# Performance work log

Measured on AMD Instinct MI355X. Metric: run time of the kernel, lower is better.

## Reference

```python
import jax, jax.numpy as jnp
import numpy as np

L, B, E = 2048, 4, 1024
H = 8
D1 = 2048          # expand_ratio * E, multiple of H
HD = D1 // H       # head dim 256
MAX_L = 2048
EPS = 1e-8


def setup_inputs() -> dict:
    key = jax.random.key(0)
    ks = jax.random.split(key, 9)
    std = 0.02
    return {
        "x": jax.random.normal(ks[0], (L, B, E), jnp.float32),
        "Wu": jax.random.normal(ks[1], (D1, E), jnp.float32) * std,
        "bu": jax.random.normal(ks[2], (D1,), jnp.float32) * std,
        "Wv": jax.random.normal(ks[3], (D1, E), jnp.float32) * std,
        "bv": jax.random.normal(ks[4], (D1,), jnp.float32) * std,
        "Wo": jax.random.normal(ks[5], (E, D1), jnp.float32) * std,
        "bo": jax.random.normal(ks[6], (E,), jnp.float32) * std,
        "zero": jax.random.normal(ks[7], (H, 1), jnp.float32) * 0.1,   # Toeplitz coef, offset 0
        "pos": jax.random.normal(ks[8], (H, MAX_L - 1), jnp.float32) * 0.1,  # offsets 1..n-1
    }


def _simple_rmsnorm(x):
    d = x.shape[-1]
    rms = jnp.linalg.norm(x, axis=-1, keepdims=True) * (d ** -0.5)
    return x / (rms + EPS)


def _toeplitz_causal_fft(v, zero, pos):
    # v: (b, h, n, hd); causal Toeplitz mixing along n via FFT long conv
    n = v.shape[-2]
    coef = jnp.concatenate([zero, pos[:, : n - 1]], axis=-1)  # (h, n)
    m = 2 * n
    cf = jnp.fft.rfft(coef, m, axis=-1)                  # (h, m//2+1)
    vf = jnp.fft.rfft(v, m, axis=-2)                     # (b, h, m//2+1, hd)
    out = jnp.fft.irfft(cf[None, :, :, None] * vf, m, axis=-2)
    return out[:, :, :n, :]


def reference(x, Wu, bu, Wv, bv, Wo, bo, zero, pos):
    # x: (n, b, e) fairseq layout
    n, b, e = x.shape
    shortcut = x
    xn = _simple_rmsnorm(x)                               # pre_norm (SimpleRMSNorm, no params)
    u = jax.nn.silu(jnp.einsum('nbe,de->nbd', xn, Wu) + bu)   # (n,b,d1)
    v = jax.nn.silu(jnp.einsum('nbe,de->nbd', xn, Wv) + bv)   # (n,b,d1)
    # 'n b (h d) -> b h n d'
    vh = v.transpose(1, 0, 2).reshape(b, n, H, HD).transpose(0, 2, 1, 3)
    oh = _toeplitz_causal_fft(vh, zero, pos)              # (b,h,n,hd)
    o = oh.transpose(0, 2, 1, 3).reshape(b, n, D1).transpose(1, 0, 2)  # (n,b,d1)
    o = u * o                                             # gating
    out = jnp.einsum('nbd,ed->nbe', o, Wo) + bo + shortcut
    return out
```

## Files before the change

kernel.cpp:

```cpp
#include <hip/hip_runtime.h>
#include <cstdint>
#include <cstddef>

#define LQ   2048
#define BQ   4
#define EQ   1024
#define HQ   8
#define D1Q  2048
#define HDQ  256
#define NBQ  (LQ*BQ)

typedef __bf16 bf16_t;
typedef __bf16 bf16x8 __attribute__((ext_vector_type(8)));
typedef __bf16 bf16x4 __attribute__((ext_vector_type(4)));
typedef float  f32x4  __attribute__((ext_vector_type(4)));

#define GAS1(p) ((const __attribute__((address_space(1))) void*)(p))
#define LAS3(p) ((__attribute__((address_space(3))) void*)(p))


__global__ __launch_bounds__(256) void convert_kernel(
    const float* __restrict__ Wu, const float* __restrict__ Wv,
    const float* __restrict__ Wo,
    bf16_t* __restrict__ Wub, bf16_t* __restrict__ Wvb,
    bf16_t* __restrict__ Wob)
{
    const size_t i = (size_t)blockIdx.x * 256 + threadIdx.x;
    if (i < (size_t)D1Q * EQ) {
        Wub[i] = (bf16_t)Wu[i];
        Wvb[i] = (bf16_t)Wv[i];
        Wob[i] = (bf16_t)Wo[i];
    }
}

__global__ __launch_bounds__(256) void build_toep_tiles(
    const float* __restrict__ zero, const float* __restrict__ pos,
    bf16_t* __restrict__ Atiles)
{
    const int q = blockIdx.x;
    const int h = blockIdx.y;
    const int doff = (q - 3) * 32;
    const int tid = threadIdx.x;
    bf16_t* dst = Atiles + ((size_t)h * 64 + q) * (128 * 32);
    const int e0 = tid * 16;
    const int r = e0 >> 5;
    const int cbase = e0 & 31;
    bf16_t vals[16];
    #pragma unroll
    for (int j = 0; j < 16; ++j) {
        const int d = doff + r - (cbase + j);
        float v = 0.f;
        if (d == 0) v = zero[h];
        else if (d > 0) v = pos[(size_t)h * (LQ - 1) + d - 1];
        vals[j] = (bf16_t)v;
    }
    *(bf16x8*)(dst + e0)     = *(bf16x8*)(vals);
    *(bf16x8*)(dst + e0 + 8) = *(bf16x8*)(vals + 8);
}

__global__ __launch_bounds__(256) void rmsnorm_kernel(
    const float* __restrict__ x, bf16_t* __restrict__ xn)
{
    const int row = blockIdx.x;
    const int tid = threadIdx.x;
    const float4 v = ((const float4*)(x + (size_t)row * EQ))[tid];
    float ss = v.x*v.x + v.y*v.y + v.z*v.z + v.w*v.w;
    #pragma unroll
    for (int m = 32; m >= 1; m >>= 1) ss += __shfl_xor(ss, m, 64);
    __shared__ float red[4];
    const int wid = tid >> 6, lane = tid & 63;
    if (lane == 0) red[wid] = ss;
    __syncthreads();
    const float tot = red[0] + red[1] + red[2] + red[3];
    const float inv = 1.f / (sqrtf(tot * (1.f / EQ)) + 1e-8f);
    bf16x4 o;
    o[0] = (bf16_t)(v.x * inv); o[1] = (bf16_t)(v.y * inv);
    o[2] = (bf16_t)(v.z * inv); o[3] = (bf16_t)(v.w * inv);
    *(bf16x4*)(xn + (size_t)row * EQ + tid * 4) = o;
}


template<int MI, int WM, int WN, int MODE, int WPB>
__global__ __launch_bounds__(512, WPB) void gemm_p(
    const bf16_t* __restrict__ A, const bf16_t* __restrict__ Bm,
    int K, int N,
    const float* __restrict__ bias, const float* __restrict__ res,
    bf16_t* __restrict__ Cb, float* __restrict__ Cf)
{
    constexpr int BM = WM * MI * 16;
    constexpr int BN = WN * 64;
    constexpr int ABYTES = BM * 64;
    constexpr int BBYTES = BN * 64;
    constexpr int BSTRIDE = ABYTES + BBYTES;
    constexpr int CB = BN / 128;
    static_assert(BM == 256, "staging assumes BM=256");
    static_assert(MODE != 1 || (MI == 8 && WN == 4), "MODE1 geometry");
    __shared__ alignas(16) char smem[3 * BSTRIDE];

    const int nwg   = gridDim.x * gridDim.y;
    const int bid0  = blockIdx.y * gridDim.x + blockIdx.x;
    const int chunkw = nwg >> 3;
    const int sb    = (bid0 & 7) * chunkw + (bid0 >> 3);
    const int bx    = sb % gridDim.x;
    const int by    = sb / gridDim.x;

    const int tid  = threadIdx.x;
    const int wid  = tid >> 6;
    const int lane = tid & 63;
    const int frow = lane & 15;
    const int c    = lane >> 4;
    const int m0 = by * BM;
    const int n0 = bx * BN;
    const int wm = wid / WN, wn = wid % WN;
    const int wrm = wm * (MI * 16);
    const int wrn = wn * 64;

    const int g = (frow >> 1) & 3;
    const int offA0 = (wrm + frow) * 64 + ((c ^ g) << 4);
    const int offB0 = ABYTES + (wrn + frow) * 64 + ((c ^ g) << 4);

    const int rA   = tid >> 2;
    const int soff = (((tid & 3) ^ ((rA >> 1) & 3)) << 4);
    const size_t lda2 = (size_t)K * 2;
    const char* sA = (const char*)A  + (size_t)(m0 + rA) * lda2 + soff;
    const char* sB = (const char*)Bm + (size_t)(n0 + rA) * lda2 + soff;

    auto STAGE = [&](int bf, int kt) {
        char* dA = smem + bf * BSTRIDE + wid * 1024;
        __builtin_amdgcn_global_load_lds(GAS1(sA + (size_t)kt * 64), LAS3(dA), 16, 0, 0);
        __builtin_amdgcn_global_load_lds(GAS1(sA + 128 * lda2 + (size_t)kt * 64),
                                         LAS3(dA + 8192), 16, 0, 0);
        char* dB = smem + bf * BSTRIDE + ABYTES + wid * 1024;
        __builtin_amdgcn_global_load_lds(GAS1(sB + (size_t)kt * 64), LAS3(dB), 16, 0, 0);
        if constexpr (CB == 2)
            __builtin_amdgcn_global_load_lds(GAS1(sB + 128 * lda2 + (size_t)kt * 64),
                                             LAS3(dB + 8192), 16, 0, 0);
    };

    f32x4 acc[MI][4];
    #pragma unroll
    for (int i = 0; i < MI; ++i)
        #pragma unroll
        for (int j = 0; j < 4; ++j) acc[i][j] = (f32x4){0.f, 0.f, 0.f, 0.f};

    const int NT = K >> 5;

    STAGE(0, 0); STAGE(1, 1);
    if constexpr (CB == 1) asm volatile("s_waitcnt vmcnt(3)" ::: "memory");
    else                   asm volatile("s_waitcnt vmcnt(4)" ::: "memory");
    __builtin_amdgcn_s_barrier();

    int cur = 0, pb = 2;
    for (int t = 0; t < NT; ++t) {
        const char* base = smem + cur * BSTRIDE;
        bf16x8 av[MI], bv[4];
        #pragma unroll
        for (int i = 0; i < MI; ++i)
            av[i] = *(const bf16x8*)(base + offA0 + i * 1024);
        #pragma unroll
        for (int i = 0; i < 4; ++i)
            bv[i] = *(const bf16x8*)(base + offB0 + i * 1024);
        if (t + 2 < NT) STAGE(pb, t + 2);
        __builtin_amdgcn_s_setprio(1);
        #pragma unroll
        for (int mi = 0; mi < MI; ++mi)
            #pragma unroll
            for (int ni = 0; ni < 4; ++ni)
                acc[mi][ni] = __builtin_amdgcn_mfma_f32_16x16x32_bf16(
                    av[mi], bv[ni], acc[mi][ni], 0, 0, 0);
        __builtin_amdgcn_s_setprio(0);
        if (t + 1 < NT) {
            if (t + 2 < NT) {
                if constexpr (CB == 1) asm volatile("s_waitcnt vmcnt(3)" ::: "memory");
                else                   asm volatile("s_waitcnt vmcnt(4)" ::: "memory");
            } else {
                asm volatile("s_waitcnt vmcnt(0)" ::: "memory");
            }
            __builtin_amdgcn_s_barrier();
        }
        cur = (cur == 2) ? 0 : cur + 1;
        pb  = (pb  == 2) ? 0 : pb  + 1;
    }

    if constexpr (MODE == 1) {
        const int hh = n0 >> 8;
        float bb[4];
        #pragma unroll
        for (int ni = 0; ni < 4; ++ni) bb[ni] = bias[n0 + wrn + ni * 16 + frow];

        #pragma unroll
        for (int p = 0; p < 2; ++p) {
            __syncthreads();
            bf16_t* chunk = (bf16_t*)smem + wid * 4224;
            #pragma unroll
            for (int mi = 0; mi < 8; ++mi) {
                #pragma unroll
                for (int nio = 0; nio < 2; ++nio) {
                    const int ni = p * 2 + nio;
                    const int nl = nio * 16 + frow;
                    #pragma unroll
                    for (int j = 0; j < 4; ++j) {
                        float v = acc[mi][ni][j] + bb[ni];
                        v = v / (1.f + __expf(-v));
                        chunk[nl * 132 + j * 32 + mi * 4 + c] = (bf16_t)v;
                    }
                }
            }
            __syncthreads();
            const int nl  = lane & 31;
            const int bh2 = lane >> 5;
            const int hd  = wrn + p * 32 + nl;
            const int t0  = (m0 + wrm) >> 2;
            #pragma unroll
            for (int bi = 0; bi < 2; ++bi) {
                const int b2 = bh2 * 2 + bi;
                const bf16_t* src = chunk + nl * 132 + b2 * 32;
                bf16_t* dst = Cb + (((size_t)hh * 4 + b2) * 256 + hd) * (size_t)LQ + t0;
                #pragma unroll
                for (int q = 0; q < 4; ++q)
                    *(bf16x8*)(dst + q * 8) = *(const bf16x8*)(src + q * 8);
            }
        }
        return;
    }

    const int fq = c * 4;
    #pragma unroll
    for (int mi = 0; mi < MI; ++mi) {
        #pragma unroll
        for (int ni = 0; ni < 4; ++ni) {
            const int gn = n0 + wrn + ni * 16 + frow;
            #pragma unroll
            for (int j = 0; j < 4; ++j) {
                const int gm = m0 + wrm + mi * 16 + fq + j;
                float v = acc[mi][ni][j];
                if constexpr (MODE == 0) {
                    v += bias[gn];
                    v = v / (1.f + __expf(-v));
                    Cb[(size_t)gm * N + gn] = (bf16_t)v;
                } else {
                    v += bias[gn] + res[(size_t)gm * N + gn];
                    Cf[(size_t)gm * N + gn] = v;
                }
            }
        }
    }
}

__global__ __launch_bounds__(512, 2) void gemm_toep_p(
    const bf16_t* __restrict__ VT, const bf16_t* __restrict__ Atiles,
    const bf16_t* __restrict__ U, bf16_t* __restrict__ O)
{
    constexpr int ABYTES = 8192;
    constexpr int BSTRIDE = ABYTES + 16384;
    __shared__ alignas(16) char smem[3 * BSTRIDE];

    const int bid   = blockIdx.x;
    const int m_blk = 15 - (bid >> 5);
    const int sub   = bid & 31;
    const int h     = sub >> 2;
    const int n0    = (sub & 3) * 256;
    const int m0    = m_blk * 128;

    const int tid  = threadIdx.x;
    const int wid  = tid >> 6;
    const int lane = tid & 63;
    const int frow = lane & 15;
    const int c    = lane >> 4;
    const int wrm  = (wid >> 2) * 64;
    const int wrn  = (wid & 3) * 64;

    const int g = (frow >> 1) & 3;
    const int offA0 = (wrm + frow) * 64 + ((c ^ g) << 4);
    const int offB0 = ABYTES + (wrn + frow) * 64 + ((c ^ g) << 4);

    const int rA   = tid >> 2;
    const int soff = (((tid & 3) ^ ((rA >> 1) & 3)) << 4);
    const char* Ah = (const char*)Atiles + (size_t)h * 64 * 8192;
    const size_t ldb = (size_t)LQ * 2;
    const char* sB = (const char*)VT + ((size_t)h * 1024 + n0 + rA) * ldb + soff;

    auto STAGE = [&](int bf, int kt) {
        const int q = 4 * m_blk + 3 - kt;
        __builtin_amdgcn_global_load_lds(
            GAS1(Ah + (size_t)q * 8192 + (size_t)rA * 64 + soff),
            LAS3(smem + bf * BSTRIDE + wid * 1024), 16, 0, 0);
        char* dB = smem + bf * BSTRIDE + ABYTES + wid * 1024;
        __builtin_amdgcn_global_load_lds(GAS1(sB + (size_t)kt * 64), LAS3(dB), 16, 0, 0);
        __builtin_amdgcn_global_load_lds(GAS1(sB + 128 * ldb + (size_t)kt * 64),
                                         LAS3(dB + 8192), 16, 0, 0);
    };

    f32x4 acc[4][4];
    #pragma unroll
    for (int i = 0; i < 4; ++i)
        #pragma unroll
        for (int j = 0; j < 4; ++j) acc[i][j] = (f32x4){0.f, 0.f, 0.f, 0.f};

    const int NT = 4 * m_blk + 4;

    STAGE(0, 0); STAGE(1, 1);
    asm volatile("s_waitcnt vmcnt(3)" ::: "memory");
    __builtin_amdgcn_s_barrier();

    int cur = 0, pb = 2;
    for (int t = 0; t < NT; ++t) {
        const char* base = smem + cur * BSTRIDE;
        bf16x8 av[4], bv[4];
        #pragma unroll
        for (int i = 0; i < 4; ++i)
            av[i] = *(const bf16x8*)(base + offA0 + i * 1024);
        #pragma unroll
        for (int i = 0; i < 4; ++i)
            bv[i] = *(const bf16x8*)(base + offB0 + i * 1024);
        if (t + 2 < NT) STAGE(pb, t + 2);
        __builtin_amdgcn_s_setprio(1);
        #pragma unroll
        for (int mi = 0; mi < 4; ++mi)
            #pragma unroll
            for (int ni = 0; ni < 4; ++ni)
                acc[mi][ni] = __builtin_amdgcn_mfma_f32_16x16x32_bf16(
                    av[mi], bv[ni], acc[mi][ni], 0, 0, 0);
        __builtin_amdgcn_s_setprio(0);
        if (t + 1 < NT) {
            if (t + 2 < NT) asm volatile("s_waitcnt vmcnt(3)" ::: "memory");
            else            asm volatile("s_waitcnt vmcnt(0)" ::: "memory");
            __builtin_amdgcn_s_barrier();
        }
        cur = (cur == 2) ? 0 : cur + 1;
        pb  = (pb  == 2) ? 0 : pb  + 1;
    }

    const int fq = c * 4;
    #pragma unroll
    for (int mi = 0; mi < 4; ++mi) {
        #pragma unroll
        for (int ni = 0; ni < 4; ++ni) {
            const int nn = n0 + wrn + ni * 16 + frow;
            const int b  = nn >> 8, hd = nn & 255;
            #pragma unroll
            for (int j = 0; j < 4; ++j) {
                const int t = m0 + wrm + mi * 16 + fq + j;
                const size_t idx = ((size_t)t * BQ + b) * D1Q + h * HDQ + hd;
                const float uval = (float)U[idx];
                O[idx] = (bf16_t)(uval * acc[mi][ni][j]);
            }
        }
    }
}


extern "C" void kernel_launch(void* const* d_in, const int* in_sizes, int n_in,
                              void* d_out, int out_size, void* d_ws, size_t ws_size,
                              hipStream_t stream)
{
    const float* x    = (const float*)d_in[0];
    const float* Wu   = (const float*)d_in[1];
    const float* bu   = (const float*)d_in[2];
    const float* Wv   = (const float*)d_in[3];
    const float* bv   = (const float*)d_in[4];
    const float* Wo   = (const float*)d_in[5];
    const float* bo   = (const float*)d_in[6];
    const float* zero = (const float*)d_in[7];
    const float* pos  = (const float*)d_in[8];
    float* out = (float*)d_out;

    char* ws = (char*)d_ws;
    size_t off = 0;
    auto alloc = [&](size_t bytes) {
        char* p = ws + off;
        off += (bytes + 255) & ~(size_t)255;
        return p;
    };
    bf16_t* xn     = (bf16_t*)alloc((size_t)NBQ * EQ * 2);
    bf16_t* Wub    = (bf16_t*)alloc((size_t)D1Q * EQ * 2);
    bf16_t* Wvb    = (bf16_t*)alloc((size_t)D1Q * EQ * 2);
    bf16_t* Wob    = (bf16_t*)alloc((size_t)EQ * D1Q * 2);
    bf16_t* Atiles = (bf16_t*)alloc((size_t)HQ * 64 * 4096 * 2);
    bf16_t* Ub     = (bf16_t*)alloc((size_t)NBQ * D1Q * 2);
    bf16_t* VTb    = (bf16_t*)alloc((size_t)NBQ * D1Q * 2);
    bf16_t* Ob     = (bf16_t*)alloc((size_t)NBQ * D1Q * 2);

    convert_kernel<<<8192, 256, 0, stream>>>(Wu, Wv, Wo, Wub, Wvb, Wob);
    build_toep_tiles<<<dim3(64, 8), 256, 0, stream>>>(zero, pos, Atiles);
    rmsnorm_kernel<<<NBQ, 256, 0, stream>>>(x, xn);

    dim3 gU(D1Q / 128, NBQ / 256);
    gemm_p<4, 4, 2, 0, 2><<<gU, 512, 0, stream>>>(xn, Wub, EQ, D1Q, bu, nullptr, Ub, nullptr);
    dim3 gV(D1Q / 256, NBQ / 256);
    gemm_p<8, 2, 4, 1, 1><<<gV, 512, 0, stream>>>(xn, Wvb, EQ, D1Q, bv, nullptr, VTb, nullptr);

    gemm_toep_p<<<512, 512, 0, stream>>>(VTb, Atiles, Ub, Ob);

    dim3 g2(EQ / 128, NBQ / 256);
    gemm_p<4, 4, 2, 2, 2><<<g2, 512, 0, stream>>>(Ob, Wob, D1Q, EQ, bo, x, nullptr, out);
}
```

Before: 206.8 us.

## Restructure GEMM pipelines with 64-wide K tiles and phased prefetch

All four GEMMs now use 64-wide K tiles with an XOR swizzle over 8 chunks. A shared phase_op helper interleaves half-tile LDS loads, asynchronous global-to-LDS staging and MFMA batches with a barrier in each phase. The U and V projections both use a new 256x256 tile kernel with two 64KB buffers. The output projection uses 128x256 tiles, and the Toeplitz tiles are rebuilt as 128x64 blocks so the causal GEMM runs half as many K-steps. The aim is to cut the barrier and waitcnt overhead per unit of MFMA work and to raise reuse per tile, at the cost of much more LDS and one block per CU.

```diff
diff --git a/kernel.cpp b/kernel.cpp
--- a/kernel.cpp
+++ b/kernel.cpp
@@ -33,29 +33,29 @@
     }
 }
 
-__global__ __launch_bounds__(256) void build_toep_tiles(
+__global__ __launch_bounds__(256) void build_toep_tiles2(
     const float* __restrict__ zero, const float* __restrict__ pos,
-    bf16_t* __restrict__ Atiles)
+    bf16_t* __restrict__ At)
 {
     const int q = blockIdx.x;
     const int h = blockIdx.y;
-    const int doff = (q - 3) * 32;
+    const int doff = (q - 1) * 64;
     const int tid = threadIdx.x;
-    bf16_t* dst = Atiles + ((size_t)h * 64 + q) * (128 * 32);
-    const int e0 = tid * 16;
-    const int r = e0 >> 5;
-    const int cbase = e0 & 31;
-    bf16_t vals[16];
-    #pragma unroll
-    for (int j = 0; j < 16; ++j) {
-        const int d = doff + r - (cbase + j);
+    bf16_t* dst = At + ((size_t)h * 32 + q) * 8192;
+    const int r  = tid >> 1;
+    const int c0 = (tid & 1) * 32;
+    bf16_t vals[32];
+    #pragma unroll
+    for (int j = 0; j < 32; ++j) {
+        const int d = doff + r - (c0 + j);
         float v = 0.f;
         if (d == 0) v = zero[h];
-        else if (d > 0) v = pos[(size_t)h * (LQ - 1) + d - 1];
+        else if (d > 0 && d < LQ) v = pos[(size_t)h * (LQ - 1) + d - 1];
         vals[j] = (bf16_t)v;
     }
-    *(bf16x8*)(dst + e0)     = *(bf16x8*)(vals);
-    *(bf16x8*)(dst + e0 + 8) = *(bf16x8*)(vals + 8);
+    #pragma unroll
+    for (int qq = 0; qq < 4; ++qq)
+        *(bf16x8*)(dst + r * 64 + c0 + qq * 8) = *(bf16x8*)(vals + qq * 8);
 }
 
 __global__ __launch_bounds__(256) void rmsnorm_kernel(
@@ -80,22 +80,42 @@
 }
 
 
-template<int MI, int WM, int WN, int MODE, int WPB>
-__global__ __launch_bounds__(512, WPB) void gemm_p(
+template<int KK, int MH, int WAITN, bool LDB, int MI_, typename F>
+__device__ __forceinline__ void phase_op(const char* base, int offA0, int offB0,
+    bf16x8 (&bv)[4], f32x4 (&acc)[MI_][4], F&& stage)
+{
+    bf16x8 av[4];
+    #pragma unroll
+    for (int i = 0; i < 4; ++i)
+        av[i] = *(const bf16x8*)(base + (offA0 ^ (KK << 6)) + (MH * 4 + i) * 2048);
+    if constexpr (LDB) {
+        #pragma unroll
+        for (int i = 0; i < 4; ++i)
+            bv[i] = *(const bf16x8*)(base + (offB0 ^ (KK << 6)) + i * 2048);
+    }
+    stage();
+    __builtin_amdgcn_s_barrier();
+    __builtin_amdgcn_s_setprio(1);
+    #pragma unroll
+    for (int i = 0; i < 4; ++i)
+        #pragma unroll
+        for (int ni = 0; ni < 4; ++ni)
+            acc[MH * 4 + i][ni] = __builtin_amdgcn_mfma_f32_16x16x32_bf16(
+                av[i], bv[ni], acc[MH * 4 + i][ni], 0, 0, 0);
+    __builtin_amdgcn_s_setprio(0);
+    if constexpr (WAITN >= 0)
+        asm volatile("s_waitcnt vmcnt(%0)" :: "i"(WAITN) : "memory");
+    __builtin_amdgcn_s_barrier();
+}
+
+
+template<int MODE>
+__global__ __launch_bounds__(512, 1) void gemm_big(
     const bf16_t* __restrict__ A, const bf16_t* __restrict__ Bm,
-    int K, int N,
-    const float* __restrict__ bias, const float* __restrict__ res,
-    bf16_t* __restrict__ Cb, float* __restrict__ Cf)
-{
-    constexpr int BM = WM * MI * 16;
-    constexpr int BN = WN * 64;
-    constexpr int ABYTES = BM * 64;
-    constexpr int BBYTES = BN * 64;
-    constexpr int BSTRIDE = ABYTES + BBYTES;
-    constexpr int CB = BN / 128;
-    static_assert(BM == 256, "staging assumes BM=256");
-    static_assert(MODE != 1 || (MI == 8 && WN == 4), "MODE1 geometry");
-    __shared__ alignas(16) char smem[3 * BSTRIDE];
+    int K, int N, const float* __restrict__ bias, bf16_t* __restrict__ Cb)
+{
+    constexpr int BSTRIDE = 65536;
+    __shared__ alignas(16) char smem[2 * BSTRIDE];
 
     const int nwg   = gridDim.x * gridDim.y;
     const int bid0  = blockIdx.y * gridDim.x + blockIdx.x;
@@ -109,77 +129,54 @@
     const int lane = tid & 63;
     const int frow = lane & 15;
     const int c    = lane >> 4;
-    const int m0 = by * BM;
-    const int n0 = bx * BN;
-    const int wm = wid / WN, wn = wid % WN;
-    const int wrm = wm * (MI * 16);
-    const int wrn = wn * 64;
-
-    const int g = (frow >> 1) & 3;
-    const int offA0 = (wrm + frow) * 64 + ((c ^ g) << 4);
-    const int offB0 = ABYTES + (wrn + frow) * 64 + ((c ^ g) << 4);
-
-    const int rA   = tid >> 2;
-    const int soff = (((tid & 3) ^ ((rA >> 1) & 3)) << 4);
+    const int m0 = by * 256;
+    const int n0 = bx * 256;
+    const int wrm = (wid >> 2) * 128;
+    const int wrn = (wid & 3) * 64;
+
+    const int g = frow & 7;
+    const int offA0 = (wrm + frow) * 128 + ((c ^ g) << 4);
+    const int offB0 = 32768 + (wrn + frow) * 128 + ((c ^ g) << 4);
+
+    const int rl = tid >> 3;
+    const int ls = (tid & 7) ^ (rl & 7);
     const size_t lda2 = (size_t)K * 2;
-    const char* sA = (const char*)A  + (size_t)(m0 + rA) * lda2 + soff;
-    const char* sB = (const char*)Bm + (size_t)(n0 + rA) * lda2 + soff;
-
-    auto STAGE = [&](int bf, int kt) {
-        char* dA = smem + bf * BSTRIDE + wid * 1024;
-        __builtin_amdgcn_global_load_lds(GAS1(sA + (size_t)kt * 64), LAS3(dA), 16, 0, 0);
-        __builtin_amdgcn_global_load_lds(GAS1(sA + 128 * lda2 + (size_t)kt * 64),
-                                         LAS3(dA + 8192), 16, 0, 0);
-        char* dB = smem + bf * BSTRIDE + ABYTES + wid * 1024;
-        __builtin_amdgcn_global_load_lds(GAS1(sB + (size_t)kt * 64), LAS3(dB), 16, 0, 0);
-        if constexpr (CB == 2)
-            __builtin_amdgcn_global_load_lds(GAS1(sB + 128 * lda2 + (size_t)kt * 64),
-                                             LAS3(dB + 8192), 16, 0, 0);
-    };
-
-    f32x4 acc[MI][4];
-    #pragma unroll
-    for (int i = 0; i < MI; ++i)
+    const char* sA = (const char*)A  + (size_t)(m0 + rl) * lda2 + ls * 16;
+    const char* sB = (const char*)Bm + (size_t)(n0 + rl) * lda2 + ls * 16;
+
+    auto SH = [&](int bf, int op, int hf, int kt) {
+        const char* s = (op ? sB : sA) + (size_t)(hf * 128) * lda2 + (size_t)kt * 128;
+        char* d = smem + bf * BSTRIDE + op * 32768 + hf * 16384 + wid * 1024;
+        __builtin_amdgcn_global_load_lds(GAS1(s), LAS3(d), 16, 0, 0);
+        __builtin_amdgcn_global_load_lds(GAS1(s + 64 * lda2), LAS3(d + 8192), 16, 0, 0);
+    };
+
+    f32x4 acc[8][4];
+    #pragma unroll
+    for (int i = 0; i < 8; ++i)
         #pragma unroll
         for (int j = 0; j < 4; ++j) acc[i][j] = (f32x4){0.f, 0.f, 0.f, 0.f};
-
-    const int NT = K >> 5;
-
-    STAGE(0, 0); STAGE(1, 1);
-    if constexpr (CB == 1) asm volatile("s_waitcnt vmcnt(3)" ::: "memory");
-    else                   asm volatile("s_waitcnt vmcnt(4)" ::: "memory");
+    bf16x8 bv[4];
+
+    const int NT = K >> 6;
+
+    SH(0,0,0,0); SH(0,0,1,0); SH(0,1,0,0); SH(0,1,1,0); SH(1,1,0,1);
+    asm volatile("s_waitcnt vmcnt(2)" ::: "memory");
     __builtin_amdgcn_s_barrier();
 
-    int cur = 0, pb = 2;
-    for (int t = 0; t < NT; ++t) {
-        const char* base = smem + cur * BSTRIDE;
-        bf16x8 av[MI], bv[4];
-        #pragma unroll
-        for (int i = 0; i < MI; ++i)
-            av[i] = *(const bf16x8*)(base + offA0 + i * 1024);
-        #pragma unroll
-        for (int i = 0; i < 4; ++i)
-            bv[i] = *(const bf16x8*)(base + offB0 + i * 1024);
-        if (t + 2 < NT) STAGE(pb, t + 2);
-        __builtin_amdgcn_s_setprio(1);
-        #pragma unroll
-        for (int mi = 0; mi < MI; ++mi)
-            #pragma unroll
-            for (int ni = 0; ni < 4; ++ni)
-                acc[mi][ni] = __builtin_amdgcn_mfma_f32_16x16x32_bf16(
-                    av[mi], bv[ni], acc[mi][ni], 0, 0, 0);
-        __builtin_amdgcn_s_setprio(0);
-        if (t + 1 < NT) {
-            if (t + 2 < NT) {
-                if constexpr (CB == 1) asm volatile("s_waitcnt vmcnt(3)" ::: "memory");
-                else                   asm volatile("s_waitcnt vmcnt(4)" ::: "memory");
-            } else {
-                asm volatile("s_waitcnt vmcnt(0)" ::: "memory");
-            }
-            __builtin_amdgcn_s_barrier();
-        }
-        cur = (cur == 2) ? 0 : cur + 1;
-        pb  = (pb  == 2) ? 0 : pb  + 1;
+    const char* b0 = smem;
+    const char* b1 = smem + BSTRIDE;
+    for (int i = 0; i < NT / 2; ++i) {
+        const int t1 = 2 * i + 1, t2 = 2 * i + 2;
+        const bool p2 = t2 < NT, p3 = t2 + 1 < NT;
+        phase_op<0,0,-1,true >(b0, offA0, offB0, bv, acc, [&]{ SH(1,1,1,t1); });
+        phase_op<0,1,-1,false>(b0, offA0, offB0, bv, acc, [&]{ SH(1,0,0,t1); });
+        phase_op<1,0,-1,true >(b0, offA0, offB0, bv, acc, [&]{ SH(1,0,1,t1); });
+        phase_op<1,1, 2,false>(b0, offA0, offB0, bv, acc, [&]{ if (p2) SH(0,1,0,t2); });
+        phase_op<0,0,-1,true >(b1, offA0, offB0, bv, acc, [&]{ if (p2) SH(0,1,1,t2); });
+        phase_op<0,1,-1,false>(b1, offA0, offB0, bv, acc, [&]{ if (p2) SH(0,0,0,t2); });
+        phase_op<1,0,-1,true >(b1, offA0, offB0, bv, acc, [&]{ if (p2) SH(0,0,1,t2); });
+        phase_op<1,1, 2,false>(b1, offA0, offB0, bv, acc, [&]{ if (p3) SH(1,1,0,t2+1); });
     }
 
     if constexpr (MODE == 1) {
@@ -226,33 +223,118 @@
 
     const int fq = c * 4;
     #pragma unroll
-    for (int mi = 0; mi < MI; ++mi) {
+    for (int mi = 0; mi < 8; ++mi) {
         #pragma unroll
         for (int ni = 0; ni < 4; ++ni) {
             const int gn = n0 + wrn + ni * 16 + frow;
             #pragma unroll
             for (int j = 0; j < 4; ++j) {
                 const int gm = m0 + wrm + mi * 16 + fq + j;
-                float v = acc[mi][ni][j];
-                if constexpr (MODE == 0) {
-                    v += bias[gn];
-                    v = v / (1.f + __expf(-v));
-                    Cb[(size_t)gm * N + gn] = (bf16_t)v;
-                } else {
-                    v += bias[gn] + res[(size_t)gm * N + gn];
-                    Cf[(size_t)gm * N + gn] = v;
-                }
+                float v = acc[mi][ni][j] + bias[gn];
+                v = v / (1.f + __expf(-v));
+                Cb[(size_t)gm * N + gn] = (bf16_t)v;
             }
         }
     }
 }
 
-__global__ __launch_bounds__(512, 2) void gemm_toep_p(
-    const bf16_t* __restrict__ VT, const bf16_t* __restrict__ Atiles,
+__global__ __launch_bounds__(512, 1) void gemm_fin(
+    const bf16_t* __restrict__ A, const bf16_t* __restrict__ Bm,
+    const float* __restrict__ bias, const float* __restrict__ res,
+    float* __restrict__ Cf)
+{
+    constexpr int K = D1Q, N = EQ;
+    constexpr int BSTRIDE = 49152;
+    __shared__ alignas(16) char smem[3 * BSTRIDE];
+
+    const int nwg   = gridDim.x * gridDim.y;
+    const int bid0  = blockIdx.y * gridDim.x + blockIdx.x;
+    const int chunkw = nwg >> 3;
+    const int sb    = (bid0 & 7) * chunkw + (bid0 >> 3);
+    const int bx    = sb % gridDim.x;
+    const int by    = sb / gridDim.x;
+
+    const int tid  = threadIdx.x;
+    const int wid  = tid >> 6;
+    const int lane = tid & 63;
+    const int frow = lane & 15;
+    const int c    = lane >> 4;
+    const int m0 = by * 128;
+    const int n0 = bx * 256;
+    const int wrm = (wid >> 2) * 64;
+    const int wrn = (wid & 3) * 64;
+
+    const int g = frow & 7;
+    const int offA0 = (wrm + frow) * 128 + ((c ^ g) << 4);
+    const int offB0 = 16384 + (wrn + frow) * 128 + ((c ^ g) << 4);
+
+    const int rl = tid >> 3;
+    const int ls = (tid & 7) ^ (rl & 7);
+    const size_t lda2 = (size_t)K * 2;
+    const char* sA = (const char*)A  + (size_t)(m0 + rl) * lda2 + ls * 16;
+    const char* sB = (const char*)Bm + (size_t)(n0 + rl) * lda2 + ls * 16;
+
+    auto SH_A = [&](int bf, int kt) {
+        const char* s = sA + (size_t)kt * 128;
+        char* d = smem + bf * BSTRIDE + wid * 1024;
+        __builtin_amdgcn_global_load_lds(GAS1(s), LAS3(d), 16, 0, 0);
+        __builtin_amdgcn_global_load_lds(GAS1(s + 64 * lda2), LAS3(d + 8192), 16, 0, 0);
+    };
+    auto SH_B = [&](int bf, int hf, int kt) {
+        const char* s = sB + (size_t)(hf * 128) * lda2 + (size_t)kt * 128;
+        char* d = smem + bf * BSTRIDE + 16384 + hf * 16384 + wid * 1024;
+        __builtin_amdgcn_global_load_lds(GAS1(s), LAS3(d), 16, 0, 0);
+        __builtin_amdgcn_global_load_lds(GAS1(s + 64 * lda2), LAS3(d + 8192), 16, 0, 0);
+    };
+
+    f32x4 acc[4][4];
+    #pragma unroll
+    for (int i = 0; i < 4; ++i)
+        #pragma unroll
+        for (int j = 0; j < 4; ++j) acc[i][j] = (f32x4){0.f, 0.f, 0.f, 0.f};
+    bf16x8 bv[4];
+
+    const int NT = K >> 6;
+
+    SH_A(0, 0); SH_B(0, 0, 0); SH_B(0, 1, 0);
+    SH_A(1, 1); SH_B(1, 0, 1); SH_B(1, 1, 1);
+    asm volatile("s_waitcnt vmcnt(6)" ::: "memory");
+    __builtin_amdgcn_s_barrier();
+
+    int cur = 0, pb = 2;
+    for (int t = 0; t < NT; ++t) {
+        const char* base = smem + cur * BSTRIDE;
+        const int t2 = t + 2;
+        const bool pf = t2 < NT;
+        phase_op<0,0,-1,true>(base, offA0, offB0, bv, acc,
+            [&]{ if (pf) { SH_A(pb, t2); SH_B(pb, 0, t2); } });
+        phase_op<1,0, 6,true>(base, offA0, offB0, bv, acc,
+            [&]{ if (pf) SH_B(pb, 1, t2); });
+        cur = (cur == 2) ? 0 : cur + 1;
+        pb  = (pb  == 2) ? 0 : pb  + 1;
+    }
+
+    const int fq = c * 4;
+    #pragma unroll
+    for (int mi = 0; mi < 4; ++mi) {
+        #pragma unroll
+        for (int ni = 0; ni < 4; ++ni) {
+            const int gn = n0 + wrn + ni * 16 + frow;
+            #pragma unroll
+            for (int j = 0; j < 4; ++j) {
+                const int gm = m0 + wrm + mi * 16 + fq + j;
+                Cf[(size_t)gm * N + gn] =
+                    acc[mi][ni][j] + bias[gn] + res[(size_t)gm * N + gn];
+            }
+        }
+    }
+}
+
+__global__ __launch_bounds__(512, 1) void gemm_toep4p(
+    const bf16_t* __restrict__ VT, const bf16_t* __restrict__ Atl,
     const bf16_t* __restrict__ U, bf16_t* __restrict__ O)
 {
-    constexpr int ABYTES = 8192;
-    constexpr int BSTRIDE = ABYTES + 16384;
+    constexpr int BSTRIDE = 49152;
     __shared__ alignas(16) char smem[3 * BSTRIDE];
 
     const int bid   = blockIdx.x;
@@ -270,25 +352,28 @@
     const int wrm  = (wid >> 2) * 64;
     const int wrn  = (wid & 3) * 64;
 
-    const int g = (frow >> 1) & 3;
-    const int offA0 = (wrm + frow) * 64 + ((c ^ g) << 4);
-    const int offB0 = ABYTES + (wrn + frow) * 64 + ((c ^ g) << 4);
-
-    const int rA   = tid >> 2;
-    const int soff = (((tid & 3) ^ ((rA >> 1) & 3)) << 4);
-    const char* Ah = (const char*)Atiles + (size_t)h * 64 * 8192;
+    const int g = frow & 7;
+    const int offA0 = (wrm + frow) * 128 + ((c ^ g) << 4);
+    const int offB0 = 16384 + (wrn + frow) * 128 + ((c ^ g) << 4);
+
+    const int rl = tid >> 3;
+    const int ls = (tid & 7) ^ (rl & 7);
+    const char* Ah = (const char*)Atl + (size_t)h * 32 * 16384;
     const size_t ldb = (size_t)LQ * 2;
-    const char* sB = (const char*)VT + ((size_t)h * 1024 + n0 + rA) * ldb + soff;
-
-    auto STAGE = [&](int bf, int kt) {
-        const int q = 4 * m_blk + 3 - kt;
-        __builtin_amdgcn_global_load_lds(
-            GAS1(Ah + (size_t)q * 8192 + (size_t)rA * 64 + soff),
-            LAS3(smem + bf * BSTRIDE + wid * 1024), 16, 0, 0);
-        char* dB = smem + bf * BSTRIDE + ABYTES + wid * 1024;
-        __builtin_amdgcn_global_load_lds(GAS1(sB + (size_t)kt * 64), LAS3(dB), 16, 0, 0);
-        __builtin_amdgcn_global_load_lds(GAS1(sB + 128 * ldb + (size_t)kt * 64),
-                                         LAS3(dB + 8192), 16, 0, 0);
+    const char* sB = (const char*)VT + ((size_t)h * 1024 + n0 + rl) * ldb + ls * 16;
+
+    auto SH_A = [&](int bf, int kt) {
+        const int q = 2 * m_blk - kt + 1;
+        const char* s = Ah + (size_t)q * 16384 + (size_t)rl * 128 + ls * 16;
+        char* d = smem + bf * BSTRIDE + wid * 1024;
+        __builtin_amdgcn_global_load_lds(GAS1(s), LAS3(d), 16, 0, 0);
+        __builtin_amdgcn_global_load_lds(GAS1(s + 64 * 128), LAS3(d + 8192), 16, 0, 0);
+    };
+    auto SH_B = [&](int bf, int hf, int kt) {
+        const char* s = sB + (size_t)(hf * 128) * ldb + (size_t)kt * 128;
+        char* d = smem + bf * BSTRIDE + 16384 + hf * 16384 + wid * 1024;
+        __builtin_amdgcn_global_load_lds(GAS1(s), LAS3(d), 16, 0, 0);
+        __builtin_amdgcn_global_load_lds(GAS1(s + 64 * ldb), LAS3(d + 8192), 16, 0, 0);
     };
 
     f32x4 acc[4][4];
@@ -296,37 +381,24 @@
     for (int i = 0; i < 4; ++i)
         #pragma unroll
         for (int j = 0; j < 4; ++j) acc[i][j] = (f32x4){0.f, 0.f, 0.f, 0.f};
-
-    const int NT = 4 * m_blk + 4;
-
-    STAGE(0, 0); STAGE(1, 1);
-    asm volatile("s_waitcnt vmcnt(3)" ::: "memory");
+    bf16x8 bv[4];
+
+    const int NT = 2 * m_blk + 2;
+
+    SH_A(0, 0); SH_B(0, 0, 0); SH_B(0, 1, 0);
+    SH_A(1, 1); SH_B(1, 0, 1); SH_B(1, 1, 1);
+    asm volatile("s_waitcnt vmcnt(6)" ::: "memory");
     __builtin_amdgcn_s_barrier();
 
     int cur = 0, pb = 2;
     for (int t = 0; t < NT; ++t) {
         const char* base = smem + cur * BSTRIDE;
-        bf16x8 av[4], bv[4];
-        #pragma unroll
-        for (int i = 0; i < 4; ++i)
-            av[i] = *(const bf16x8*)(base + offA0 + i * 1024);
-        #pragma unroll
-        for (int i = 0; i < 4; ++i)
-            bv[i] = *(const bf16x8*)(base + offB0 + i * 1024);
-        if (t + 2 < NT) STAGE(pb, t + 2);
-        __builtin_amdgcn_s_setprio(1);
-        #pragma unroll
-        for (int mi = 0; mi < 4; ++mi)
-            #pragma unroll
-            for (int ni = 0; ni < 4; ++ni)
-                acc[mi][ni] = __builtin_amdgcn_mfma_f32_16x16x32_bf16(
-                    av[mi], bv[ni], acc[mi][ni], 0, 0, 0);
-        __builtin_amdgcn_s_setprio(0);
-        if (t + 1 < NT) {
-            if (t + 2 < NT) asm volatile("s_waitcnt vmcnt(3)" ::: "memory");
-            else            asm volatile("s_waitcnt vmcnt(0)" ::: "memory");
-            __builtin_amdgcn_s_barrier();
-        }
+        const int t2 = t + 2;
+        const bool pf = t2 < NT;
+        phase_op<0,0,-1,true>(base, offA0, offB0, bv, acc,
+            [&]{ if (pf) { SH_A(pb, t2); SH_B(pb, 0, t2); } });
+        phase_op<1,0, 6,true>(base, offA0, offB0, bv, acc,
+            [&]{ if (pf) SH_B(pb, 1, t2); });
         cur = (cur == 2) ? 0 : cur + 1;
         pb  = (pb  == 2) ? 0 : pb  + 1;
     }
@@ -376,22 +448,21 @@
     bf16_t* Wub    = (bf16_t*)alloc((size_t)D1Q * EQ * 2);
     bf16_t* Wvb    = (bf16_t*)alloc((size_t)D1Q * EQ * 2);
     bf16_t* Wob    = (bf16_t*)alloc((size_t)EQ * D1Q * 2);
-    bf16_t* Atiles = (bf16_t*)alloc((size_t)HQ * 64 * 4096 * 2);
+    bf16_t* Atiles = (bf16_t*)alloc((size_t)HQ * 32 * 8192 * 2);
     bf16_t* Ub     = (bf16_t*)alloc((size_t)NBQ * D1Q * 2);
     bf16_t* VTb    = (bf16_t*)alloc((size_t)NBQ * D1Q * 2);
     bf16_t* Ob     = (bf16_t*)alloc((size_t)NBQ * D1Q * 2);
 
     convert_kernel<<<8192, 256, 0, stream>>>(Wu, Wv, Wo, Wub, Wvb, Wob);
-    build_toep_tiles<<<dim3(64, 8), 256, 0, stream>>>(zero, pos, Atiles);
+    build_toep_tiles2<<<dim3(32, 8), 256, 0, stream>>>(zero, pos, Atiles);
     rmsnorm_kernel<<<NBQ, 256, 0, stream>>>(x, xn);
 
-    dim3 gU(D1Q / 128, NBQ / 256);
-    gemm_p<4, 4, 2, 0, 2><<<gU, 512, 0, stream>>>(xn, Wub, EQ, D1Q, bu, nullptr, Ub, nullptr);
-    dim3 gV(D1Q / 256, NBQ / 256);
-    gemm_p<8, 2, 4, 1, 1><<<gV, 512, 0, stream>>>(xn, Wvb, EQ, D1Q, bv, nullptr, VTb, nullptr);
-
-    gemm_toep_p<<<512, 512, 0, stream>>>(VTb, Atiles, Ub, Ob);
-
-    dim3 g2(EQ / 128, NBQ / 256);
-    gemm_p<4, 4, 2, 2, 2><<<g2, 512, 0, stream>>>(Ob, Wob, D1Q, EQ, bo, x, nullptr, out);
-}
+    dim3 g1(D1Q / 256, NBQ / 256);
+    gemm_big<0><<<g1, 512, 0, stream>>>(xn, Wub, EQ, D1Q, bu, Ub);
+    gemm_big<1><<<g1, 512, 0, stream>>>(xn, Wvb, EQ, D1Q, bv, VTb);
+
+    gemm_toep4p<<<512, 512, 0, stream>>>(VTb, Atiles, Ub, Ob);
+
+    dim3 g2(EQ / 256, NBQ / 128);
+    gemm_fin<<<g2, 512, 0, stream>>>(Ob, Wob, bo, x, out);
+}
```

Measured after the change: 198.2 us. 4.2% less time.

## Merge U/V projections into one GEMM launch and shrink tiles with double buffering

Applied to the files above, without the earlier changes.

The two input-projection GEMMs become a single launch. Its grid spans both weight matrices, relying on Wvb sitting contiguously after Wub in the workspace, and the epilogue branches per block to write either gated U or transposed V. The Toeplitz and output GEMMs move from 512-thread 256-wide tiles to 256-thread 128x128 tiles, doubling the number of blocks and raising the occupancy hint. All GEMMs switch from a three-stage LDS pipeline to two stages with a full vmcnt(0) wait every iteration. This aims for better load balance and more resident blocks, at the cost of shallower prefetch and more redundant operand loads from the smaller tiles.

```diff
diff --git a/kernel.cpp b/kernel.cpp
--- a/kernel.cpp
+++ b/kernel.cpp
@@ -79,23 +79,14 @@
     *(bf16x4*)(xn + (size_t)row * EQ + tid * 4) = o;
 }
 
-
-template<int MI, int WM, int WN, int MODE, int WPB>
-__global__ __launch_bounds__(512, WPB) void gemm_p(
+__global__ __launch_bounds__(512, 4) void gemm_uv(
     const bf16_t* __restrict__ A, const bf16_t* __restrict__ Bm,
-    int K, int N,
-    const float* __restrict__ bias, const float* __restrict__ res,
-    bf16_t* __restrict__ Cb, float* __restrict__ Cf)
-{
-    constexpr int BM = WM * MI * 16;
-    constexpr int BN = WN * 64;
-    constexpr int ABYTES = BM * 64;
-    constexpr int BBYTES = BN * 64;
-    constexpr int BSTRIDE = ABYTES + BBYTES;
-    constexpr int CB = BN / 128;
-    static_assert(BM == 256, "staging assumes BM=256");
-    static_assert(MODE != 1 || (MI == 8 && WN == 4), "MODE1 geometry");
-    __shared__ alignas(16) char smem[3 * BSTRIDE];
+    const float* __restrict__ bbu, const float* __restrict__ bbv,
+    bf16_t* __restrict__ Ub, bf16_t* __restrict__ Vt)
+{
+    constexpr int K = EQ;
+    constexpr int BUF = 24576;
+    __shared__ alignas(16) char smem[2 * BUF];
 
     const int nwg   = gridDim.x * gridDim.y;
     const int bid0  = blockIdx.y * gridDim.x + blockIdx.x;
@@ -109,15 +100,14 @@
     const int lane = tid & 63;
     const int frow = lane & 15;
     const int c    = lane >> 4;
-    const int m0 = by * BM;
-    const int n0 = bx * BN;
-    const int wm = wid / WN, wn = wid % WN;
-    const int wrm = wm * (MI * 16);
-    const int wrn = wn * 64;
+    const int m0 = by * 256;
+    const int n0 = bx * 128;
+    const int wm = wid >> 1, wn = wid & 1;
+    const int wrm = wm * 64, wrn = wn * 64;
 
     const int g = (frow >> 1) & 3;
     const int offA0 = (wrm + frow) * 64 + ((c ^ g) << 4);
-    const int offB0 = ABYTES + (wrn + frow) * 64 + ((c ^ g) << 4);
+    const int offB0 = 16384 + (wrn + frow) * 64 + ((c ^ g) << 4);
 
     const int rA   = tid >> 2;
     const int soff = (((tid & 3) ^ ((rA >> 1) & 3)) << 4);
@@ -126,140 +116,120 @@
     const char* sB = (const char*)Bm + (size_t)(n0 + rA) * lda2 + soff;
 
     auto STAGE = [&](int bf, int kt) {
-        char* dA = smem + bf * BSTRIDE + wid * 1024;
+        char* dA = smem + bf * BUF + wid * 1024;
         __builtin_amdgcn_global_load_lds(GAS1(sA + (size_t)kt * 64), LAS3(dA), 16, 0, 0);
         __builtin_amdgcn_global_load_lds(GAS1(sA + 128 * lda2 + (size_t)kt * 64),
                                          LAS3(dA + 8192), 16, 0, 0);
-        char* dB = smem + bf * BSTRIDE + ABYTES + wid * 1024;
+        char* dB = smem + bf * BUF + 16384 + wid * 1024;
         __builtin_amdgcn_global_load_lds(GAS1(sB + (size_t)kt * 64), LAS3(dB), 16, 0, 0);
-        if constexpr (CB == 2)
-            __builtin_amdgcn_global_load_lds(GAS1(sB + 128 * lda2 + (size_t)kt * 64),
-                                             LAS3(dB + 8192), 16, 0, 0);
     };
 
-    f32x4 acc[MI][4];
-    #pragma unroll
-    for (int i = 0; i < MI; ++i)
+    f32x4 acc[4][4];
+    #pragma unroll
+    for (int i = 0; i < 4; ++i)
         #pragma unroll
         for (int j = 0; j < 4; ++j) acc[i][j] = (f32x4){0.f, 0.f, 0.f, 0.f};
 
     const int NT = K >> 5;
 
-    STAGE(0, 0); STAGE(1, 1);
-    if constexpr (CB == 1) asm volatile("s_waitcnt vmcnt(3)" ::: "memory");
-    else                   asm volatile("s_waitcnt vmcnt(4)" ::: "memory");
+    STAGE(0, 0);
+    asm volatile("s_waitcnt vmcnt(0)" ::: "memory");
     __builtin_amdgcn_s_barrier();
 
-    int cur = 0, pb = 2;
     for (int t = 0; t < NT; ++t) {
-        const char* base = smem + cur * BSTRIDE;
-        bf16x8 av[MI], bv[4];
-        #pragma unroll
-        for (int i = 0; i < MI; ++i)
+        if (t + 1 < NT) STAGE((t + 1) & 1, t + 1);
+        const char* base = smem + (t & 1) * BUF;
+        bf16x8 av[4], bv[4];
+        #pragma unroll
+        for (int i = 0; i < 4; ++i) {
             av[i] = *(const bf16x8*)(base + offA0 + i * 1024);
-        #pragma unroll
-        for (int i = 0; i < 4; ++i)
             bv[i] = *(const bf16x8*)(base + offB0 + i * 1024);
-        if (t + 2 < NT) STAGE(pb, t + 2);
+        }
         __builtin_amdgcn_s_setprio(1);
         #pragma unroll
-        for (int mi = 0; mi < MI; ++mi)
+        for (int mi = 0; mi < 4; ++mi)
             #pragma unroll
             for (int ni = 0; ni < 4; ++ni)
                 acc[mi][ni] = __builtin_amdgcn_mfma_f32_16x16x32_bf16(
                     av[mi], bv[ni], acc[mi][ni], 0, 0, 0);
         __builtin_amdgcn_s_setprio(0);
-        if (t + 1 < NT) {
-            if (t + 2 < NT) {
-                if constexpr (CB == 1) asm volatile("s_waitcnt vmcnt(3)" ::: "memory");
-                else                   asm volatile("s_waitcnt vmcnt(4)" ::: "memory");
-            } else {
-                asm volatile("s_waitcnt vmcnt(0)" ::: "memory");
+        asm volatile("s_waitcnt vmcnt(0)" ::: "memory");
+        __builtin_amdgcn_s_barrier();
+    }
+
+    if (bx < 16) {
+        const int fq = c * 4;
+        #pragma unroll
+        for (int mi = 0; mi < 4; ++mi) {
+            #pragma unroll
+            for (int ni = 0; ni < 4; ++ni) {
+                const int gn = n0 + wrn + ni * 16 + frow;
+                #pragma unroll
+                for (int j = 0; j < 4; ++j) {
+                    const int gm = m0 + wrm + mi * 16 + fq + j;
+                    float v = acc[mi][ni][j] + bbu[gn];
+                    v = v / (1.f + __expf(-v));
+                    Ub[(size_t)gm * D1Q + gn] = (bf16_t)v;
+                }
             }
-            __builtin_amdgcn_s_barrier();
-        }
-        cur = (cur == 2) ? 0 : cur + 1;
-        pb  = (pb  == 2) ? 0 : pb  + 1;
-    }
-
-    if constexpr (MODE == 1) {
-        const int hh = n0 >> 8;
+        }
+        return;
+    }
+
+    {
+        const int n0v = n0 - 2048;
+        const int hh  = n0v >> 8;
+        const int hdb = (n0v & 255) + wrn;
         float bb[4];
         #pragma unroll
-        for (int ni = 0; ni < 4; ++ni) bb[ni] = bias[n0 + wrn + ni * 16 + frow];
-
+        for (int ni = 0; ni < 4; ++ni) bb[ni] = bbv[n0v + wrn + ni * 16 + frow];
+
+        bf16_t* chunk = (bf16_t*)smem + wn * 8448;
         #pragma unroll
         for (int p = 0; p < 2; ++p) {
             __syncthreads();
-            bf16_t* chunk = (bf16_t*)smem + wid * 4224;
-            #pragma unroll
-            for (int mi = 0; mi < 8; ++mi) {
+            #pragma unroll
+            for (int mi = 0; mi < 4; ++mi) {
                 #pragma unroll
                 for (int nio = 0; nio < 2; ++nio) {
                     const int ni = p * 2 + nio;
                     const int nl = nio * 16 + frow;
+                    const int tl = wm * 16 + mi * 4 + c;
                     #pragma unroll
                     for (int j = 0; j < 4; ++j) {
                         float v = acc[mi][ni][j] + bb[ni];
                         v = v / (1.f + __expf(-v));
-                        chunk[nl * 132 + j * 32 + mi * 4 + c] = (bf16_t)v;
+                        chunk[nl * 264 + j * 64 + tl] = (bf16_t)v;
                     }
                 }
             }
             __syncthreads();
-            const int nl  = lane & 31;
-            const int bh2 = lane >> 5;
-            const int hd  = wrn + p * 32 + nl;
-            const int t0  = (m0 + wrm) >> 2;
-            #pragma unroll
-            for (int bi = 0; bi < 2; ++bi) {
-                const int b2 = bh2 * 2 + bi;
-                const bf16_t* src = chunk + nl * 132 + b2 * 32;
-                bf16_t* dst = Cb + (((size_t)hh * 4 + b2) * 256 + hd) * (size_t)LQ + t0;
-                #pragma unroll
-                for (int q = 0; q < 4; ++q)
-                    *(bf16x8*)(dst + q * 8) = *(const bf16x8*)(src + q * 8);
-            }
-        }
-        return;
-    }
-
-    const int fq = c * 4;
-    #pragma unroll
-    for (int mi = 0; mi < MI; ++mi) {
-        #pragma unroll
-        for (int ni = 0; ni < 4; ++ni) {
-            const int gn = n0 + wrn + ni * 16 + frow;
-            #pragma unroll
-            for (int j = 0; j < 4; ++j) {
-                const int gm = m0 + wrm + mi * 16 + fq + j;
-                float v = acc[mi][ni][j];
-                if constexpr (MODE == 0) {
-                    v += bias[gn];
-                    v = v / (1.f + __expf(-v));
-                    Cb[(size_t)gm * N + gn] = (bf16_t)v;
-                } else {
-                    v += bias[gn] + res[(size_t)gm * N + gn];
-                    Cf[(size_t)gm * N + gn] = v;
-                }
-            }
-        }
-    }
-}
-
-__global__ __launch_bounds__(512, 2) void gemm_toep_p(
+            const int nl    = lane & 31;
+            const int thalf = lane >> 5;
+            const int b2    = wm;
+            const int hd    = hdb + p * 32 + nl;
+            const int t0    = (m0 >> 2) + thalf * 32;
+            const bf16_t* src = chunk + nl * 264 + b2 * 64 + thalf * 32;
+            bf16_t* dst = Vt + (((size_t)hh * 4 + b2) * 256 + hd) * (size_t)LQ + t0;
+            #pragma unroll
+            for (int u = 0; u < 4; ++u)
+                *(bf16x8*)(dst + u * 8) = *(const bf16x8*)(src + u * 8);
+        }
+    }
+}
+
+__global__ __launch_bounds__(256, 4) void gemm_toep(
     const bf16_t* __restrict__ VT, const bf16_t* __restrict__ Atiles,
     const bf16_t* __restrict__ U, bf16_t* __restrict__ O)
 {
-    constexpr int ABYTES = 8192;
-    constexpr int BSTRIDE = ABYTES + 16384;
-    __shared__ alignas(16) char smem[3 * BSTRIDE];
+    constexpr int BUF = 16384;
+    __shared__ alignas(16) char smem[2 * BUF];
 
     const int bid   = blockIdx.x;
-    const int m_blk = 15 - (bid >> 5);
-    const int sub   = bid & 31;
-    const int h     = sub >> 2;
-    const int n0    = (sub & 3) * 256;
+    const int m_blk = 15 - (bid >> 6);
+    const int sub   = bid & 63;
+    const int h     = sub >> 3;
+    const int n0    = (sub & 7) * 128;
     const int m0    = m_blk * 128;
 
     const int tid  = threadIdx.x;
@@ -267,12 +237,12 @@
     const int lane = tid & 63;
     const int frow = lane & 15;
     const int c    = lane >> 4;
-    const int wrm  = (wid >> 2) * 64;
-    const int wrn  = (wid & 3) * 64;
+    const int wm = wid >> 1, wn = wid & 1;
+    const int wrm = wm * 64, wrn = wn * 64;
 
     const int g = (frow >> 1) & 3;
     const int offA0 = (wrm + frow) * 64 + ((c ^ g) << 4);
-    const int offB0 = ABYTES + (wrn + frow) * 64 + ((c ^ g) << 4);
+    const int offB0 = 8192 + (wrn + frow) * 64 + ((c ^ g) << 4);
 
     const int rA   = tid >> 2;
     const int soff = (((tid & 3) ^ ((rA >> 1) & 3)) << 4);
@@ -282,13 +252,14 @@
 
     auto STAGE = [&](int bf, int kt) {
         const int q = 4 * m_blk + 3 - kt;
-        __builtin_amdgcn_global_load_lds(
-            GAS1(Ah + (size_t)q * 8192 + (size_t)rA * 64 + soff),
-            LAS3(smem + bf * BSTRIDE + wid * 1024), 16, 0, 0);
-        char* dB = smem + bf * BSTRIDE + ABYTES + wid * 1024;
+        const char* s = Ah + (size_t)q * 8192 + (size_t)rA * 64 + soff;
+        char* dA = smem + bf * BUF + wid * 1024;
+        __builtin_amdgcn_global_load_lds(GAS1(s), LAS3(dA), 16, 0, 0);
+        __builtin_amdgcn_global_load_lds(GAS1(s + 4096), LAS3(dA + 4096), 16, 0, 0);
+        char* dB = smem + bf * BUF + 8192 + wid * 1024;
         __builtin_amdgcn_global_load_lds(GAS1(sB + (size_t)kt * 64), LAS3(dB), 16, 0, 0);
-        __builtin_amdgcn_global_load_lds(GAS1(sB + 128 * ldb + (size_t)kt * 64),
-                                         LAS3(dB + 8192), 16, 0, 0);
+        __builtin_amdgcn_global_load_lds(GAS1(sB + 64 * ldb + (size_t)kt * 64),
+                                         LAS3(dB + 4096), 16, 0, 0);
     };
 
     f32x4 acc[4][4];
@@ -299,21 +270,19 @@
 
     const int NT = 4 * m_blk + 4;
 
-    STAGE(0, 0); STAGE(1, 1);
-    asm volatile("s_waitcnt vmcnt(3)" ::: "memory");
+    STAGE(0, 0);
+    asm volatile("s_waitcnt vmcnt(0)" ::: "memory");
     __builtin_amdgcn_s_barrier();
 
-    int cur = 0, pb = 2;
     for (int t = 0; t < NT; ++t) {
-        const char* base = smem + cur * BSTRIDE;
+        if (t + 1 < NT) STAGE((t + 1) & 1, t + 1);
+        const char* base = smem + (t & 1) * BUF;
         bf16x8 av[4], bv[4];
         #pragma unroll
-        for (int i = 0; i < 4; ++i)
+        for (int i = 0; i < 4; ++i) {
             av[i] = *(const bf16x8*)(base + offA0 + i * 1024);
-        #pragma unroll
-        for (int i = 0; i < 4; ++i)
             bv[i] = *(const bf16x8*)(base + offB0 + i * 1024);
-        if (t + 2 < NT) STAGE(pb, t + 2);
+        }
         __builtin_amdgcn_s_setprio(1);
         #pragma unroll
         for (int mi = 0; mi < 4; ++mi)
@@ -322,13 +291,8 @@
                 acc[mi][ni] = __builtin_amdgcn_mfma_f32_16x16x32_bf16(
                     av[mi], bv[ni], acc[mi][ni], 0, 0, 0);
         __builtin_amdgcn_s_setprio(0);
-        if (t + 1 < NT) {
-            if (t + 2 < NT) asm volatile("s_waitcnt vmcnt(3)" ::: "memory");
-            else            asm volatile("s_waitcnt vmcnt(0)" ::: "memory");
-            __builtin_amdgcn_s_barrier();
-        }
-        cur = (cur == 2) ? 0 : cur + 1;
-        pb  = (pb  == 2) ? 0 : pb  + 1;
+        asm volatile("s_waitcnt vmcnt(0)" ::: "memory");
+        __builtin_amdgcn_s_barrier();
     }
 
     const int fq = c * 4;
@@ -344,6 +308,102 @@
                 const size_t idx = ((size_t)t * BQ + b) * D1Q + h * HDQ + hd;
                 const float uval = (float)U[idx];
                 O[idx] = (bf16_t)(uval * acc[mi][ni][j]);
+            }
+        }
+    }
+}
+
+__global__ __launch_bounds__(256, 4) void gemm_fin(
+    const bf16_t* __restrict__ A, const bf16_t* __restrict__ Bm,
+    const float* __restrict__ bias, const float* __restrict__ res,
+    float* __restrict__ Cf)
+{
+    constexpr int K = D1Q, N = EQ;
+    constexpr int BUF = 16384;
+    __shared__ alignas(16) char smem[2 * BUF];
+
+    const int nwg   = gridDim.x * gridDim.y;
+    const int bid0  = blockIdx.y * gridDim.x + blockIdx.x;
+    const int chunkw = nwg >> 3;
+    const int sb    = (bid0 & 7) * chunkw + (bid0 >> 3);
+    const int bx    = sb % gridDim.x;
+    const int by    = sb / gridDim.x;
+
+    const int tid  = threadIdx.x;
+    const int wid  = tid >> 6;
+    const int lane = tid & 63;
+    const int frow = lane & 15;
+    const int c    = lane >> 4;
+    const int m0 = by * 128;
+    const int n0 = bx * 128;
+    const int wm = wid >> 1, wn = wid & 1;
+    const int wrm = wm * 64, wrn = wn * 64;
+
+    const int g = (frow >> 1) & 3;
+    const int offA0 = (wrm + frow) * 64 + ((c ^ g) << 4);
+    const int offB0 = 8192 + (wrn + frow) * 64 + ((c ^ g) << 4);
+
+    const int rA   = tid >> 2;
+    const int soff = (((tid & 3) ^ ((rA >> 1) & 3)) << 4);
+    const size_t lda2 = (size_t)K * 2;
+    const char* sA = (const char*)A  + (size_t)(m0 + rA) * lda2 + soff;
+    const char* sB = (const char*)Bm + (size_t)(n0 + rA) * lda2 + soff;
+
+    auto STAGE = [&](int bf, int kt) {
+        char* dA = smem + bf * BUF + wid * 1024;
+        __builtin_amdgcn_global_load_lds(GAS1(sA + (size_t)kt * 64), LAS3(dA), 16, 0, 0);
+        __builtin_amdgcn_global_load_lds(GAS1(sA + 64 * lda2 + (size_t)kt * 64),
+                                         LAS3(dA + 4096), 16, 0, 0);
+        char* dB = smem + bf * BUF + 8192 + wid * 1024;
+        __builtin_amdgcn_global_load_lds(GAS1(sB + (size_t)kt * 64), LAS3(dB), 16, 0, 0);
+        __builtin_amdgcn_global_load_lds(GAS1(sB + 64 * lda2 + (size_t)kt * 64),
+                                         LAS3(dB + 4096), 16, 0, 0);
+    };
+
+    f32x4 acc[4][4];
+    #pragma unroll
+    for (int i = 0; i < 4; ++i)
+        #pragma unroll
+        for (int j = 0; j < 4; ++j) acc[i][j] = (f32x4){0.f, 0.f, 0.f, 0.f};
+
+    const int NT = K >> 5;
+
+    STAGE(0, 0);
+    asm volatile("s_waitcnt vmcnt(0)" ::: "memory");
+    __builtin_amdgcn_s_barrier();
+
+    for (int t = 0; t < NT; ++t) {
+        if (t + 1 < NT) STAGE((t + 1) & 1, t + 1);
+        const char* base = smem + (t & 1) * BUF;
+        bf16x8 av[4], bv[4];
+        #pragma unroll
+        for (int i = 0; i < 4; ++i) {
+            av[i] = *(const bf16x8*)(base + offA0 + i * 1024);
+            bv[i] = *(const bf16x8*)(base + offB0 + i * 1024);
+        }
+        __builtin_amdgcn_s_setprio(1);
+        #pragma unroll
+        for (int mi = 0; mi < 4; ++mi)
+            #pragma unroll
+            for (int ni = 0; ni < 4; ++ni)
+                acc[mi][ni] = __builtin_amdgcn_mfma_f32_16x16x32_bf16(
+                    av[mi], bv[ni], acc[mi][ni], 0, 0, 0);
+        __builtin_amdgcn_s_setprio(0);
+        asm volatile("s_waitcnt vmcnt(0)" ::: "memory");
+        __builtin_amdgcn_s_barrier();
+    }
+
+    const int fq = c * 4;
+    #pragma unroll
+    for (int mi = 0; mi < 4; ++mi) {
+        #pragma unroll
+        for (int ni = 0; ni < 4; ++ni) {
+            const int gn = n0 + wrn + ni * 16 + frow;
+            #pragma unroll
+            for (int j = 0; j < 4; ++j) {
+                const int gm = m0 + wrm + mi * 16 + fq + j;
+                Cf[(size_t)gm * N + gn] =
+                    acc[mi][ni][j] + bias[gn] + res[(size_t)gm * N + gn];
             }
         }
     }
@@ -385,13 +445,11 @@
     build_toep_tiles<<<dim3(64, 8), 256, 0, stream>>>(zero, pos, Atiles);
     rmsnorm_kernel<<<NBQ, 256, 0, stream>>>(x, xn);
 
-    dim3 gU(D1Q / 128, NBQ / 256);
-    gemm_p<4, 4, 2, 0, 2><<<gU, 512, 0, stream>>>(xn, Wub, EQ, D1Q, bu, nullptr, Ub, nullptr);
-    dim3 gV(D1Q / 256, NBQ / 256);
-    gemm_p<8, 2, 4, 1, 1><<<gV, 512, 0, stream>>>(xn, Wvb, EQ, D1Q, bv, nullptr, VTb, nullptr);
-
-    gemm_toep_p<<<512, 512, 0, stream>>>(VTb, Atiles, Ub, Ob);
-
-    dim3 g2(EQ / 128, NBQ / 256);
-    gemm_p<4, 4, 2, 2, 2><<<g2, 512, 0, stream>>>(Ob, Wob, D1Q, EQ, bo, x, nullptr, out);
-}
+    dim3 g1(32, NBQ / 256);
+    gemm_uv<<<g1, 512, 0, stream>>>(xn, Wub, bu, bv, Ub, VTb);
+
+    gemm_toep<<<1024, 256, 0, stream>>>(VTb, Atiles, Ub, Ob);
+
+    dim3 g2(EQ / 128, NBQ / 128);
+    gemm_fin<<<g2, 256, 0, stream>>>(Ob, Wob, bo, x, out);
+}
```

After: 200.2 us. 1.03x faster.
